# Performance work log

Hardware: AMD Instinct MI355X
Metric: run time of the kernel (lower is better)

The kernel has to match this reference:

```python
import jax, jax.numpy as jnp
import numpy as np

K = 3        # kernel_size
EPS = 1e-4   # eps from __init__


def _conv_valid(x, w):
    # NHWC input, HWIO filter, VALID padding, stride 1
    return jax.lax.conv_general_dilated(
        x, w, window_strides=(1, 1), padding='VALID',
        dimension_numbers=('NHWC', 'HWIO', 'NHWC'))


def _backward_standardize_weight(grad_in, original_weights, gain, w_max_bitmap, eps):
    # Faithful translation of BackwardInjectWSConv2D.backward_standardize_weight
    kh, kw, cin, cout = original_weights.shape
    N = float(kh * kw * cin)                       # b*h*w in the TF code
    mu = jnp.mean(original_weights, axis=(0, 1, 2))
    xmu = original_weights - mu                    # [K,K,Cin,Cout]
    var = jnp.mean(jnp.square(xmu), axis=(0, 1, 2))
    mvar = N * var
    maxvar = jnp.maximum(mvar, eps)
    sqrtvar = jnp.sqrt(maxvar)
    ivar = 1.0 / sqrtvar
    givar = gain * ivar                            # [Cout]
    dgivar = jnp.sum(grad_in * xmu, axis=(0, 1, 2))
    divar = dgivar * gain
    dgain = dgivar * ivar
    dxmu1 = grad_in * givar
    dsqrtvar = (-1.0 / jnp.square(sqrtvar)) * divar
    dmaxvar = (0.5 / jnp.sqrt(maxvar)) * dsqrtvar
    dmvar = w_max_bitmap * dmaxvar
    dvar = N * dmvar
    dsq = (1.0 / N) * dvar                         # (1/N)*ones_like(grad_in)*dvar, broadcast
    dxmu2 = 2.0 * xmu * dsq
    dx1 = dxmu1 + dxmu2
    dmu = -jnp.sum(dx1, axis=(0, 1, 2))
    dx2 = (1.0 / N) * dmu                          # broadcast over [K,K,Cin]
    dx = dx1 + dx2
    return dx, dgain


def setup_inputs() -> dict:
    key = jax.random.key(0)
    ks = jax.random.split(key, 5)
    B, H, W, Cin, Cout = 64, 56, 56, 128, 128
    return {
        'grad_output': jax.random.normal(ks[0], (B, H, W, Cout), jnp.float32),
        'inputs': jax.random.normal(ks[1], (B, H, W, Cin), jnp.float32),
        'kernels': jax.random.normal(ks[2], (K, K, Cin, Cout), jnp.float32),
        'std_kernels': jax.random.normal(ks[3], (K, K, Cin, Cout), jnp.float32),
        'gain': jax.random.uniform(ks[4], (Cout,), jnp.float32),
        'w_max_bitmap': jnp.ones((Cout,), jnp.float32),
    }


def reference(grad_output, inputs, kernels, std_kernels, gain, w_max_bitmap):
    pad = (K - 1) // 2
    # ---- grad wrt input: full conv of grad_out with rot180(std_kernels), io swapped
    go_pad = jnp.pad(grad_output, ((0, 0), (pad, pad), (pad, pad), (0, 0)))
    w_rot = jnp.transpose(std_kernels[::-1, ::-1], (0, 1, 3, 2))   # [K,K,Cout,Cin]
    manual_grad_in = _conv_valid(go_pad, w_rot)                    # [B,H,W,Cin]
    # ---- grad wrt weight: treat Cin as batch, B as contraction channel
    in_pad = jnp.pad(inputs, ((0, 0), (pad, pad), (pad, pad), (0, 0)))
    fmt_inp = jnp.transpose(in_pad, (3, 1, 2, 0))                  # [Cin,H+2p,W+2p,B]
    fmt_wt = jnp.transpose(grad_output, (1, 2, 0, 3))              # [H,W,B,Cout]
    direct = _conv_valid(fmt_inp, fmt_wt)                          # [Cin,K,K,Cout]
    grad_wt_raw = jnp.transpose(direct, (1, 2, 0, 3))              # [K,K,Cin,Cout]
    # ---- weight-standardization backward chain
    manual_grad_wt, manual_grad_gain = _backward_standardize_weight(
        grad_wt_raw, kernels, gain, w_max_bitmap, EPS)
    # ---- bias grad
    manual_grad_bias = jnp.sum(grad_output, axis=(0, 1, 2))        # [Cout]
    return manual_grad_in, manual_grad_wt, manual_grad_bias, manual_grad_gain
```

## Files before the change

### kernel.cpp

```cpp
#include <hip/hip_runtime.h>
#include <hip/hip_bf16.h>

typedef __bf16 bf16x8 __attribute__((ext_vector_type(8)));
typedef __bf16 bf16x4 __attribute__((ext_vector_type(4)));
typedef float  f32x4  __attribute__((ext_vector_type(4)));
typedef unsigned int u32;

#define HW_   3136
#define NPIX  200704
#define GI_ELEMS 25690112

#define GOT_OFF   0u
#define RAW_OFF   51380224u
#define BIASA_OFF 51970048u
#define STDKF_OFF 51970560u
#define GUARD_OFF 52265472u
#define ZB_OFF    52265728u
#define ZA_OFF    52272000u
#define X_OFF     52279168u

__device__ __forceinline__ f32x4 mfma16(bf16x8 a, bf16x8 b, f32x4 c){
  return __builtin_amdgcn_mfma_f32_16x16x32_bf16(a, b, c, 0, 0, 0);
}

__device__ __forceinline__ void async16(const void* g, __bf16* l){
  __builtin_amdgcn_global_load_lds(
      (const __attribute__((address_space(1))) void*)g,
      (__attribute__((address_space(3))) void*)l, 16, 0, 0);
}

__global__ __launch_bounds__(256) void k_prep(const float* __restrict__ s, __bf16* __restrict__ d){
  const int g = blockIdx.x*256 + threadIdx.x;
  const int l = g & 63;
  const int j = (g >> 6) & 7;
  const int kc = (g >> 9) & 3;
  const int tap = g >> 11;
  const int ci = j*16 + (l & 15);
  const int co0 = kc*32 + (l >> 4)*8;
  const float* src = s + ((size_t)(tap*128 + ci))*128 + co0;
  f32x4 x0 = *(const f32x4*)src;
  f32x4 x1 = *(const f32x4*)(src + 4);
  bf16x8 y;
  #pragma unroll
  for (int e=0;e<4;e++){ y[e] = (__bf16)x0[e]; y[e+4] = (__bf16)x1[e]; }
  *(bf16x8*)(d + (size_t)g*8) = y;
}

__global__ __launch_bounds__(256) void k_goT(const float* __restrict__ go,
                                             __bf16* __restrict__ goT,
                                             __bf16* __restrict__ goB,
                                             float* __restrict__ biasA){
  __shared__ __bf16 T[64][130];
  __shared__ float biasS[128];
  const int t = threadIdx.x;
  const size_t p0 = (size_t)blockIdx.x*64;
  if (t < 128) biasS[t] = 0.f;
  __syncthreads();
  float bs[4] = {0.f,0.f,0.f,0.f};
  const int co0 = (t*4) & 127;
  #pragma unroll
  for (int i=0;i<8;i++){
    const int flat = (i*256+t)*4;
    const int px = flat >> 7, co = flat & 127;
    f32x4 x = *(const f32x4*)(go + p0*128 + flat);
    bf16x4 y;
    #pragma unroll
    for (int e=0;e<4;e++){ y[e] = (__bf16)x[e]; bs[e] += x[e]; }
    *(bf16x4*)&T[px][co] = y;
    *(bf16x4*)(goB + p0*128 + flat) = y;
  }
  #pragma unroll
  for (int e=0;e<4;e++) atomicAdd(&biasS[co0+e], bs[e]);
  __syncthreads();
  #pragma unroll
  for (int j=0;j<2;j++){
    const int task = j*256 + t;
    const int co = task >> 2, q = task & 3;
    bf16x8 v0, v1;
    #pragma unroll
    for (int k=0;k<8;k++) v0[k] = T[q*16+k][co];
    #pragma unroll
    for (int k=0;k<8;k++) v1[k] = T[q*16+8+k][co];
    __bf16* d = goT + (size_t)co*NPIX + p0 + q*16;
    *(bf16x8*)d = v0; *(bf16x8*)(d+8) = v1;
  }
  if (t < 128) atomicAdd(&biasA[t], biasS[t]);
}

__global__ __launch_bounds__(256) void k_inT(const float* __restrict__ inp,
                                             __bf16* __restrict__ inT){
  __shared__ __bf16 T[64][130];
  const int t = threadIdx.x;
  const size_t p0 = (size_t)blockIdx.x*64;
  #pragma unroll
  for (int i=0;i<8;i++){
    const int flat = (i*256+t)*4;
    const int px = flat >> 7, ci = flat & 127;
    f32x4 x = *(const f32x4*)(inp + p0*128 + flat);
    bf16x4 y;
    #pragma unroll
    for (int e=0;e<4;e++) y[e] = (__bf16)x[e];
    *(bf16x4*)&T[px][ci] = y;
  }
  __syncthreads();
  #pragma unroll
  for (int j=0;j<4;j++){
    const int task = j*256 + t;
    const int ci = task >> 3, ch = task & 7;
    const int p = (int)p0 + ch*8;
    const int b = p / HW_; const int r = p - b*HW_;
    const int h = r / 56;  const int w = r - h*56;
    bf16x8 v;
    #pragma unroll
    for (int k=0;k<8;k++) v[k] = T[ch*8+k][ci];
    *(bf16x8*)(inT + (((size_t)(ci*64+b))*58 + (h+1))*64 + w) = v;
  }
}

__global__ __launch_bounds__(256) void k_padz(__bf16* __restrict__ inT){
  const int g = blockIdx.x*256 + threadIdx.x;
  const int pair = g / 72, k = g - pair*72;
  __bf16* base = inT + (size_t)pair*3712;
  int off;
  if (k < 8)       off = k*8;
  else if (k < 16) off = 57*64 + (k-8)*8;
  else             off = (k-15)*64 + 56;
  bf16x8 z = {};
  *(bf16x8*)(base + off) = z;
}

__global__ __launch_bounds__(512, 2) void k_gradin4(const __bf16* __restrict__ goB,
                                                    const __bf16* __restrict__ stdkF,
                                                    const __bf16* __restrict__ zsrc,
                                                    float* __restrict__ out){
  __shared__ char LDS[148480];
  const int t = threadIdx.x;
  const int wv = t >> 6, l = t & 63, lr = l & 15, lg = l >> 4;
  const int b = blockIdx.x, h0 = blockIdx.y*8;
  const int j0 = (wv & 1)*4;
  const int pxg = (wv >> 1)*112;

  #pragma unroll
  for (int it=0; it<19; ++it){
    const int qb = it*512 + wv*64;
    if (qb < 9280){
      const u32 q = qb + l;
      const u32 r = q / 928u;
      const u32 rem = q - r*928u;
      const u32 wp = rem >> 4;
      const u32 c = rem & 15u;
      const int h = h0 - 1 + (int)r;
      const u32 s = r*58u + wp;
      const u32 csrc = c ^ (s & 7u);
      const bool valid = (h >= 0) & (h < 56) & (wp >= 1u) & (wp <= 56u);
      const __bf16* src = valid
        ? goB + ((size_t)((b*HW_) + h*56 + ((int)wp - 1))*128 + csrc*8)
        : zsrc;
      async16(src, (__bf16*)(LDS + qb*16));
    }
  }

  int sb[7];
  #pragma unroll
  for (int tile=0; tile<7; ++tile){
    const int p = pxg + tile*16 + lr;
    const int ro = p / 56; const int w = p - ro*56;
    sb[tile] = (ro + 2)*58 + (w + 2);
  }

  f32x4 acc[7][4];
  #pragma unroll
  for (int i=0;i<7;i++){
    #pragma unroll
    for (int j=0;j<4;j++){
      #pragma unroll
      for (int r=0;r<4;r++) acc[i][j][r] = 0.f;
    }
  }
  __syncthreads();

  for (int tap=0; tap<9; ++tap){
    const int u = tap/3;
    const int soff = u*58 + (tap - u*3);
    #pragma unroll
    for (int kc=0; kc<4; ++kc){
      bf16x8 Bf[4];
      #pragma unroll
      for (int j=0;j<4;++j)
        Bf[j] = *(const bf16x8*)(stdkF + ((size_t)(((tap*4 + kc)*8 + j0 + j)*64 + l))*8);
      bf16x8 Af[7];
      #pragma unroll
      for (int tile=0;tile<7;++tile){
        const int s = sb[tile] - soff;
        const int byte = (s << 8) | (((kc*4 + lg) ^ (s & 7)) << 4);
        Af[tile] = *(const bf16x8*)(LDS + byte);
      }
      #pragma unroll
      for (int tile=0;tile<7;++tile){
        #pragma unroll
        for (int j=0;j<4;++j)
          acc[tile][j] = mfma16(Af[tile], Bf[j], acc[tile][j]);
      }
    }
  }

  float* o = out + ((size_t)b*HW_ + (size_t)h0*56 + pxg)*128;
  #pragma unroll
  for (int tile=0;tile<7;++tile){
    #pragma unroll
    for (int j=0;j<4;++j){
      #pragma unroll
      for (int r=0;r<4;++r)
        o[(size_t)(tile*16 + 4*lg + r)*128 + (j0 + j)*16 + lr] = acc[tile][j][r];
    }
  }
}

#define GW_G 29696
#define GW_A 29728

__global__ __launch_bounds__(256, 2) void k_gradwt3(const char* __restrict__ ws,
                                                    float* __restrict__ raw){
  __shared__ __bf16 LDS[36000];
  const int t = threadIdx.x;
  const int w = t >> 6, l = t & 63, lr = l & 15, lg = l >> 4;
  const int b = blockIdx.x, ci0 = blockIdx.y*16;
  const int wco = w*32;

  if (t < 32) LDS[GW_G + t] = (__bf16)0.f;

  u32 boff[15];
  #pragma unroll
  for (int i=0;i<15;i++){
    const int chunk = i*256 + w*64 + l;
    const int co = chunk / 29, part = chunk - co*29;
    boff[i] = (part < 28)
      ? (GOT_OFF + (u32)(co*NPIX + b*HW_ + part*8)*2u)
      : ZB_OFF;
  }
  u32 aoff[4];
  #pragma unroll
  for (int i=0;i<4;i++){
    const int chunk = i*256 + w*64 + l;
    const int ci = chunk / 49, r = chunk - ci*49;
    aoff[i] = (r < 48)
      ? (X_OFF + (u32)((((ci0+ci)*64 + b)*58 + (r>>3))*64 + (r&7)*8)*2u)
      : ZA_OFF;
  }

  f32x4 acc[9][2];
  #pragma unroll
  for (int tp=0;tp<9;tp++){
    #pragma unroll
    for (int j=0;j<2;j++){
      #pragma unroll
      for (int r=0;r<4;r++) acc[tp][j][r] = 0.f;
    }
  }

  for (int c=0; c<14; ++c){
    #pragma unroll
    for (int i=0;i<15;i++){
      if (i < 14 || w < 2){
        async16(ws + boff[i], LDS + (i*256 + w*64)*8);
        boff[i] += 448u;
      }
    }
    #pragma unroll
    for (int i=0;i<4;i++){
      if (i < 3 || (w == 0 && l < 16)){
        async16(ws + aoff[i], LDS + GW_A + (i*256 + w*64)*8);
        aoff[i] += 512u;
      }
    }
    __syncthreads();

    const __bf16* Bb = LDS;
    const __bf16* Ab = LDS + GW_A;
    #pragma unroll
    for (int ks=0; ks<7; ++ks){
      const int pl = ks*32 + lg*8;
      const int q  = ks*4 + lg;
      const int hl = q / 7;
      const int w0 = pl - hl*56;
      bf16x8 b0 = *(const bf16x8*)&Bb[(wco + lr)*232 + pl];
      bf16x8 b1 = *(const bf16x8*)&Bb[(wco + 16 + lr)*232 + pl];
      const __bf16* abase = &Ab[lr*392 + hl*64 + w0];
      #pragma unroll
      for (int u=0; u<3; ++u){
        const __bf16* ap = abase + u*64;
        union { bf16x8 v; u32 d[4]; } va, a0, a2;
        va.v = *(const bf16x8*)ap;
        const u32 m1 = *(const unsigned short*)(ap - 1);
        const u32 p8 = *(const unsigned short*)(ap + 8);
        a0.d[0] = (va.d[0] << 16) | m1;
        a0.d[1] = (va.d[1] << 16) | (va.d[0] >> 16);
        a0.d[2] = (va.d[2] << 16) | (va.d[1] >> 16);
        a0.d[3] = (va.d[3] << 16) | (va.d[2] >> 16);
        a2.d[0] = (va.d[0] >> 16) | (va.d[1] << 16);
        a2.d[1] = (va.d[1] >> 16) | (va.d[2] << 16);
        a2.d[2] = (va.d[2] >> 16) | (va.d[3] << 16);
        a2.d[3] = (va.d[3] >> 16) | (p8 << 16);
        acc[u*3+0][0] = mfma16(a0.v, b0, acc[u*3+0][0]);
        acc[u*3+0][1] = mfma16(a0.v, b1, acc[u*3+0][1]);
        acc[u*3+1][0] = mfma16(va.v, b0, acc[u*3+1][0]);
        acc[u*3+1][1] = mfma16(va.v, b1, acc[u*3+1][1]);
        acc[u*3+2][0] = mfma16(a2.v, b0, acc[u*3+2][0]);
        acc[u*3+2][1] = mfma16(a2.v, b1, acc[u*3+2][1]);
      }
    }
    __syncthreads();
  }

  #pragma unroll
  for (int tp=0;tp<9;tp++){
    #pragma unroll
    for (int j=0;j<2;j++){
      #pragma unroll
      for (int r=0;r<4;r++)
        atomicAdd(&raw[(size_t)(tp*128 + ci0 + 4*lg + r)*128 + wco + j*16 + lr],
                  acc[tp][j][r]);
    }
  }
}

__global__ __launch_bounds__(128) void k_std(const float* __restrict__ raw,
      const float* __restrict__ kern, const float* __restrict__ gain,
      const float* __restrict__ bmap, const float* __restrict__ biasA,
      float* __restrict__ out_wt, float* __restrict__ out_bias, float* __restrict__ out_gain){
  const int co = blockIdx.x, t = threadIdx.x;
  float kv[9], gv[9];
  float s1=0.f, s2=0.f, sg=0.f, sgk=0.f;
  #pragma unroll
  for (int i=0;i<9;i++){
    const int m = t + i*128;
    const float k_ = kern[(size_t)m*128 + co];
    const float g_ = raw [(size_t)m*128 + co];
    kv[i]=k_; gv[i]=g_;
    s1 += k_; s2 += k_*k_; sg += g_; sgk += g_*k_;
  }
  __shared__ float red[4][128];
  red[0][t]=s1; red[1][t]=s2; red[2][t]=sg; red[3][t]=sgk;
  __syncthreads();
  for (int off=64; off>0; off>>=1){
    if (t < off){
      red[0][t]+=red[0][t+off]; red[1][t]+=red[1][t+off];
      red[2][t]+=red[2][t+off]; red[3][t]+=red[3][t+off];
    }
    __syncthreads();
  }
  const float N = 1152.f;
  const float S1=red[0][0], S2=red[1][0], Sg=red[2][0], Sgk=red[3][0];
  const float mu = S1/N;
  const float var = S2/N - mu*mu;
  const float mvar = N*var;
  const float maxvar = fmaxf(mvar, 1e-4f);
  const float sqrtvar = sqrtf(maxvar);
  const float ivar = 1.f/sqrtvar;
  const float g = gain[co];
  const float givar = g*ivar;
  const float dgivar = Sgk - mu*Sg;
  const float divar = dgivar*g;
  const float dsqrtvar = -divar/maxvar;
  const float dmaxvar = 0.5f*dsqrtvar/sqrtvar;
  const float dsq = bmap[co]*dmaxvar;
  const float dmu = -(givar*Sg + 2.f*dsq*(S1 - N*mu));
  const float dmuN = dmu*(1.f/N);
  #pragma unroll
  for (int i=0;i<9;i++){
    const int m = t + i*128;
    out_wt[(size_t)m*128 + co] = gv[i]*givar + 2.f*(kv[i]-mu)*dsq + dmuN;
  }
  if (t == 0){ out_gain[co] = dgivar*ivar; out_bias[co] = biasA[co]; }
}

extern "C" void kernel_launch(void* const* d_in, const int* in_sizes, int n_in,
                              void* d_out, int out_size, void* d_ws, size_t ws_size,
                              hipStream_t stream){
  const float* go   = (const float*)d_in[0];
  const float* inp  = (const float*)d_in[1];
  const float* kern = (const float*)d_in[2];
  const float* stdk = (const float*)d_in[3];
  const float* gain = (const float*)d_in[4];
  const float* bmap = (const float*)d_in[5];

  char* ws = (char*)d_ws;
  __bf16* goT   = (__bf16*)(ws + GOT_OFF);
  float*  raw   = (float*) (ws + RAW_OFF);
  float*  biasA = (float*) (ws + BIASA_OFF);
  __bf16* stdkF = (__bf16*)(ws + STDKF_OFF);
  char*   guard =           ws + GUARD_OFF;
  __bf16* goB   = (__bf16*)(ws + X_OFF);
  __bf16* inT   = (__bf16*)(ws + X_OFF);

  hipMemsetAsync(ws + RAW_OFF,   0, 589824 + 512, stream);
  hipMemsetAsync(ws + GUARD_OFF, 0, 256 + 6272 + 7168, stream);

  k_prep  <<<72, 256, 0, stream>>>(stdk, stdkF);
  k_goT   <<<3136, 256, 0, stream>>>(go, goT, goB, biasA);
  k_gradin4<<<dim3(64,7), 512, 0, stream>>>(goB, stdkF, (const __bf16*)guard, (float*)d_out);

  k_padz  <<<2304, 256, 0, stream>>>(inT);
  k_inT   <<<3136, 256, 0, stream>>>(inp, inT);
  k_gradwt3<<<dim3(64,8), 256, 0, stream>>>((const char*)ws, raw);

  float* out = (float*)d_out;
  k_std<<<128, 128, 0, stream>>>(raw, kern, gain, bmap, biasA,
                                 out + GI_ELEMS,
                                 out + GI_ELEMS + 147456,
                                 out + GI_ELEMS + 147456 + 128);
}
```

Measured before the change: 302.3 us.

## Split grad-weight K-steps across two wave groups and use shuffles for halo

The grad-weight kernel moves from 256 to 512 threads per block. The extra four waves take a disjoint subset of the seven K-steps (4 vs 3), so each block runs two partial reductions into separate accumulators that are both atomically added to the output. The staging loads are spread over twice as many threads, and the neighbouring-element halo reads come from cross-lane shuffles instead of extra LDS loads, with edge lanes still reading from LDS. This raises parallelism and latency hiding per block, at the cost of doubling the atomic traffic, an uneven 4/3 split between the wave groups, and higher register pressure under the 512-thread launch bound.

```diff
diff --git a/kernel.cpp b/kernel.cpp
--- a/kernel.cpp
+++ b/kernel.cpp
@@ -219,33 +219,75 @@
 #define GW_G 29696
 #define GW_A 29728
 
-__global__ __launch_bounds__(256, 2) void k_gradwt3(const char* __restrict__ ws,
+#define KSTEP(ks)                                                              \
+{                                                                              \
+  const int pl = (ks)*32 + lg*8;                                               \
+  const int q  = (ks)*4 + lg;                                                  \
+  const int hl = q / 7;                                                        \
+  const int w0 = pl - hl*56;                                                   \
+  bf16x8 b0 = *(const bf16x8*)&LDS[(wco + lr)*232 + pl];                       \
+  bf16x8 b1 = *(const bf16x8*)&LDS[(wco + 16 + lr)*232 + pl];                  \
+  const __bf16* abase = &LDS[GW_A + lr*392 + hl*64 + w0];                      \
+  _Pragma("unroll")                                                            \
+  for (int u=0; u<3; ++u){                                                     \
+    const __bf16* ap = abase + u*64;                                           \
+    union { bf16x8 v; u32 d[4]; } va, a0, a2;                                  \
+    va.v = *(const bf16x8*)ap;                                                 \
+    u32 m1 = ((u32)__shfl_up((int)va.d[3], 16)) >> 16;                         \
+    u32 p8 = ((u32)__shfl_down((int)va.d[0], 16)) & 0xffffu;                   \
+    if (w0 == 0)  m1 = 0;                           \
+    if (w0 == 48) p8 = 0;                            \
+    if (lg == 0) m1 = *(const unsigned short*)(ap - 1);                        \
+    if (lg == 3) p8 = *(const unsigned short*)(ap + 8);                        \
+    a0.d[0] = (va.d[0] << 16) | m1;                                            \
+    a0.d[1] = (va.d[1] << 16) | (va.d[0] >> 16);                               \
+    a0.d[2] = (va.d[2] << 16) | (va.d[1] >> 16);                               \
+    a0.d[3] = (va.d[3] << 16) | (va.d[2] >> 16);                               \
+    a2.d[0] = (va.d[0] >> 16) | (va.d[1] << 16);                               \
+    a2.d[1] = (va.d[1] >> 16) | (va.d[2] << 16);                               \
+    a2.d[2] = (va.d[2] >> 16) | (va.d[3] << 16);                               \
+    a2.d[3] = (va.d[3] >> 16) | (p8 << 16);                                    \
+    acc[u*3+0][0] = mfma16(a0.v, b0, acc[u*3+0][0]);                           \
+    acc[u*3+0][1] = mfma16(a0.v, b1, acc[u*3+0][1]);                           \
+    acc[u*3+1][0] = mfma16(va.v, b0, acc[u*3+1][0]);                           \
+    acc[u*3+1][1] = mfma16(va.v, b1, acc[u*3+1][1]);                           \
+    acc[u*3+2][0] = mfma16(a2.v, b0, acc[u*3+2][0]);                           \
+    acc[u*3+2][1] = mfma16(a2.v, b1, acc[u*3+2][1]);                           \
+  }                                                                            \
+}
+
+__global__ __launch_bounds__(512, 4) void k_gradwt5(const char* __restrict__ ws,
                                                     float* __restrict__ raw){
   __shared__ __bf16 LDS[36000];
   const int t = threadIdx.x;
-  const int w = t >> 6, l = t & 63, lr = l & 15, lg = l >> 4;
+  const int wv = t >> 6, l = t & 63, lr = l & 15, lg = l >> 4;
   const int b = blockIdx.x, ci0 = blockIdx.y*16;
-  const int wco = w*32;
+  const int wco = (wv & 3)*32;
+  const int kh = wv >> 2;
 
   if (t < 32) LDS[GW_G + t] = (__bf16)0.f;
 
-  u32 boff[15];
-  #pragma unroll
-  for (int i=0;i<15;i++){
-    const int chunk = i*256 + w*64 + l;
-    const int co = chunk / 29, part = chunk - co*29;
-    boff[i] = (part < 28)
-      ? (GOT_OFF + (u32)(co*NPIX + b*HW_ + part*8)*2u)
-      : ZB_OFF;
-  }
-  u32 aoff[4];
-  #pragma unroll
-  for (int i=0;i<4;i++){
-    const int chunk = i*256 + w*64 + l;
-    const int ci = chunk / 49, r = chunk - ci*49;
-    aoff[i] = (r < 48)
-      ? (X_OFF + (u32)((((ci0+ci)*64 + b)*58 + (r>>3))*64 + (r&7)*8)*2u)
-      : ZA_OFF;
+  u32 boff[8];
+  #pragma unroll
+  for (int i=0;i<8;i++){
+    const int chunk = i*512 + wv*64 + l;
+    if (chunk < 3712){
+      const int co = chunk / 29, part = chunk - co*29;
+      boff[i] = (part < 28)
+        ? (GOT_OFF + (u32)(co*NPIX + b*HW_ + part*8)*2u)
+        : ZB_OFF;
+    } else boff[i] = ZB_OFF;
+  }
+  u32 aoff[2];
+  #pragma unroll
+  for (int i=0;i<2;i++){
+    const int chunk = i*512 + wv*64 + l;
+    if (chunk < 784){
+      const int ci = chunk / 49, r = chunk - ci*49;
+      aoff[i] = (r < 48)
+        ? (X_OFF + (u32)((((ci0+ci)*64 + b)*58 + (r>>3))*64 + (r&7)*8)*2u)
+        : ZA_OFF;
+    } else aoff[i] = ZA_OFF;
   }
 
   f32x4 acc[9][2];
@@ -260,55 +302,27 @@
 
   for (int c=0; c<14; ++c){
     #pragma unroll
-    for (int i=0;i<15;i++){
-      if (i < 14 || w < 2){
-        async16(ws + boff[i], LDS + (i*256 + w*64)*8);
+    for (int i=0;i<8;i++){
+      const int qb = i*512 + wv*64;
+      if (qb < 3712){
+        async16(ws + boff[i], LDS + qb*8);
         boff[i] += 448u;
       }
     }
     #pragma unroll
-    for (int i=0;i<4;i++){
-      if (i < 3 || (w == 0 && l < 16)){
-        async16(ws + aoff[i], LDS + GW_A + (i*256 + w*64)*8);
+    for (int i=0;i<2;i++){
+      const int qb = i*512 + wv*64;
+      const int chunk = qb + l;
+      if (chunk < 784){
+        async16(ws + aoff[i], LDS + GW_A + qb*8);
         aoff[i] += 512u;
       }
     }
     __syncthreads();
 
-    const __bf16* Bb = LDS;
-    const __bf16* Ab = LDS + GW_A;
-    #pragma unroll
-    for (int ks=0; ks<7; ++ks){
-      const int pl = ks*32 + lg*8;
-      const int q  = ks*4 + lg;
-      const int hl = q / 7;
-      const int w0 = pl - hl*56;
-      bf16x8 b0 = *(const bf16x8*)&Bb[(wco + lr)*232 + pl];
-      bf16x8 b1 = *(const bf16x8*)&Bb[(wco + 16 + lr)*232 + pl];
-      const __bf16* abase = &Ab[lr*392 + hl*64 + w0];
-      #pragma unroll
-      for (int u=0; u<3; ++u){
-        const __bf16* ap = abase + u*64;
-        union { bf16x8 v; u32 d[4]; } va, a0, a2;
-        va.v = *(const bf16x8*)ap;
-        const u32 m1 = *(const unsigned short*)(ap - 1);
-        const u32 p8 = *(const unsigned short*)(ap + 8);
-        a0.d[0] = (va.d[0] << 16) | m1;
-        a0.d[1] = (va.d[1] << 16) | (va.d[0] >> 16);
-        a0.d[2] = (va.d[2] << 16) | (va.d[1] >> 16);
-        a0.d[3] = (va.d[3] << 16) | (va.d[2] >> 16);
-        a2.d[0] = (va.d[0] >> 16) | (va.d[1] << 16);
-        a2.d[1] = (va.d[1] >> 16) | (va.d[2] << 16);
-        a2.d[2] = (va.d[2] >> 16) | (va.d[3] << 16);
-        a2.d[3] = (va.d[3] >> 16) | (p8 << 16);
-        acc[u*3+0][0] = mfma16(a0.v, b0, acc[u*3+0][0]);
-        acc[u*3+0][1] = mfma16(a0.v, b1, acc[u*3+0][1]);
-        acc[u*3+1][0] = mfma16(va.v, b0, acc[u*3+1][0]);
-        acc[u*3+1][1] = mfma16(va.v, b1, acc[u*3+1][1]);
-        acc[u*3+2][0] = mfma16(a2.v, b0, acc[u*3+2][0]);
-        acc[u*3+2][1] = mfma16(a2.v, b1, acc[u*3+2][1]);
-      }
-    }
+    if (kh == 0){ KSTEP(0) KSTEP(1) KSTEP(2) KSTEP(3) }
+    else        { KSTEP(4) KSTEP(5) KSTEP(6) }
+
     __syncthreads();
   }
 
@@ -402,7 +416,7 @@
 
   k_padz  <<<2304, 256, 0, stream>>>(inT);
   k_inT   <<<3136, 256, 0, stream>>>(inp, inT);
-  k_gradwt3<<<dim3(64,8), 256, 0, stream>>>((const char*)ws, raw);
+  k_gradwt5<<<dim3(64,8), 512, 0, stream>>>((const char*)ws, raw);
 
   float* out = (float*)d_out;
   k_std<<<128, 128, 0, stream>>>(raw, kern, gain, bmap, biasA,
```

New measurement: 423.7 us. 1.4x slower.
